# Kernel optimization log

Measured on AMD Instinct MI355X. Metric: run time of the kernel, lower is better.

## Reference

```python
import jax, jax.numpy as jnp
import numpy as np

HEADS = 12
DIM_HEAD = 64
SCALE = DIM_HEAD ** -0.5


def rotate_every_two(x):
    # (..., 2d) -> rotate pairs: (x1, x2) -> (-x2, x1)
    x = x.reshape(*x.shape[:-1], -1, 2)
    x1, x2 = x[..., 0], x[..., 1]
    return jnp.stack((-x2, x1), axis=-1).reshape(*x.shape[:-2], -1)


def apply_rotary_pos_emb(q, k, sinu_pos):
    # sinu_pos: (b, p, 2c) -> sin, cos each (b, p, c)
    b, p, two_c = sinu_pos.shape
    sp = sinu_pos.reshape(b, p, 2, two_c // 2)
    sin, cos = sp[:, :, 0, :], sp[:, :, 1, :]
    # interleave-repeat to (b, 1, p, 2c) to broadcast over heads
    sin = jnp.repeat(sin, 2, axis=-1)[:, None, :, :]
    cos = jnp.repeat(cos, 2, axis=-1)[:, None, :, :]
    rot = lambda t: t * cos + rotate_every_two(t) * sin
    return rot(q), rot(k)


def setup_inputs() -> dict:
    key = jax.random.key(0)
    ks = jax.random.split(key, 5)
    b, n, dim = 8, 1024, 768
    inner = HEADS * DIM_HEAD
    x = jax.random.normal(ks[0], (b, n, dim), dtype=jnp.float32)
    pos_emb = jax.random.normal(ks[1], (1, n, DIM_HEAD), dtype=jnp.float32)
    W_qkv = jax.random.normal(ks[2], (dim, 3 * inner), dtype=jnp.float32) * (dim ** -0.5)
    W_out = jax.random.normal(ks[3], (inner, dim), dtype=jnp.float32) * (inner ** -0.5)
    b_out = jnp.zeros((dim,), dtype=jnp.float32)
    return {"x": x, "pos_emb": pos_emb, "W_qkv": W_qkv, "W_out": W_out, "b_out": b_out}


def reference(x, pos_emb, W_qkv, W_out, b_out):
    b, n, _ = x.shape
    qkv = x @ W_qkv                                   # (b, n, 3*inner)
    q, k, v = jnp.split(qkv, 3, axis=-1)
    split_heads = lambda t: t.reshape(b, n, HEADS, DIM_HEAD).transpose(0, 2, 1, 3)
    q, k, v = split_heads(q), split_heads(k), split_heads(v)   # (b, h, n, d)
    q, k = apply_rotary_pos_emb(q, k, pos_emb)
    dots = jnp.einsum('bhid,bhjd->bhij', q, k) * SCALE
    attn = jax.nn.softmax(dots, axis=-1)
    out = jnp.einsum('bhij,bhjd->bhid', attn, v)
    out = out.transpose(0, 2, 1, 3).reshape(b, n, HEADS * DIM_HEAD)
    out = out @ W_out + b_out
    return out  # context is None -> torch code returns (out[:, :n], None); n == full length
```

## Files before the change

kernel.cpp:

```cpp
#include <hip/hip_runtime.h>
#include <hip/hip_bf16.h>

typedef __attribute__((ext_vector_type(8))) short bf16x8;
typedef __attribute__((ext_vector_type(4))) float f32x4;
typedef __attribute__((ext_vector_type(4))) unsigned short u16x4;
typedef unsigned short u16;
typedef unsigned int u32;

#define DEVINL __device__ __forceinline__

DEVINL u16 f2bf(float f) {
    union { float f; u32 u; } v; v.f = f;
    u32 r = v.u + 0x7FFFu + ((v.u >> 16) & 1u);
    return (u16)(r >> 16);
}
DEVINL float bf2f(u16 h) {
    union { u32 u; float f; } v; v.u = ((u32)h) << 16;
    return v.f;
}
DEVINL u32 cvt_pk_bf16(float lo, float hi) {
    u32 r;
    asm("v_cvt_pk_bf16_f32 %0, %1, %2" : "=v"(r) : "v"(lo), "v"(hi));
    return r;
}

template<int Nv> DEVINL void vmcnt_asm() {
    if constexpr (Nv == 0) asm volatile("s_waitcnt vmcnt(0)" ::: "memory");
    else if constexpr (Nv == 1) asm volatile("s_waitcnt vmcnt(1)" ::: "memory");
    else if constexpr (Nv == 2) asm volatile("s_waitcnt vmcnt(2)" ::: "memory");
    else if constexpr (Nv == 3) asm volatile("s_waitcnt vmcnt(3)" ::: "memory");
    else if constexpr (Nv == 4) asm volatile("s_waitcnt vmcnt(4)" ::: "memory");
    else if constexpr (Nv == 5) asm volatile("s_waitcnt vmcnt(5)" ::: "memory");
    else if constexpr (Nv == 6) asm volatile("s_waitcnt vmcnt(6)" ::: "memory");
    else asm volatile("s_waitcnt vmcnt(7)" ::: "memory");
}

#define GLOAD_LDS16(g, l) __builtin_amdgcn_global_load_lds( \
    (const __attribute__((address_space(1))) void*)(g), \
    (__attribute__((address_space(3))) void*)(l), 16, 0, 0)

#define SBAR() do { \
    __builtin_amdgcn_sched_barrier(0); \
    __builtin_amdgcn_s_barrier(); \
    __builtin_amdgcn_sched_barrier(0); } while (0)

__global__ void cvt_bf16_kernel(const float* __restrict__ in, u16* __restrict__ out, int n4) {
    int t = blockIdx.x * blockDim.x + threadIdx.x;
    if (t >= n4) return;
    const float4 v = reinterpret_cast<const float4*>(in)[t];
    u16x4 o;
    o[0] = f2bf(v.x); o[1] = f2bf(v.y); o[2] = f2bf(v.z); o[3] = f2bf(v.w);
    *reinterpret_cast<u16x4*>(out + (size_t)t * 4) = o;
}

__global__ __launch_bounds__(256) void transpose_cvt_kernel(const float* __restrict__ in,
                                                            u16* __restrict__ out,
                                                            int R, int C) {
    __shared__ float tile[32][33];
    int c0 = blockIdx.x * 32, r0 = blockIdx.y * 32;
    int tx = threadIdx.x & 31, ty = threadIdx.x >> 5;
#pragma unroll
    for (int i = 0; i < 4; ++i)
        tile[ty + i * 8][tx] = in[(size_t)(r0 + ty + i * 8) * C + c0 + tx];
    __syncthreads();
#pragma unroll
    for (int i = 0; i < 4; ++i)
        out[(size_t)(c0 + ty + i * 8) * R + r0 + tx] = f2bf(tile[tx][ty + i * 8]);
}

template<int NTN, int NFRAG, int BROWS, int K, bool BF16_OUT>
__global__ __launch_bounds__(512, 2) void gemm_bigtile_kernel(const u16* __restrict__ A,
                                                              const u16* __restrict__ Bt,
                                                              void* __restrict__ Cout,
                                                              const float* __restrict__ bias) {
    constexpr int BN = NFRAG * 32;
    constexpr int N = NTN * BN;
    constexpr int NT = K / 64;
    constexpr int PA = 256 * 32;
    constexpr int PB = BROWS * 32;
    constexpr int PKS = PA + PB;
    constexpr int PBUF = 2 * PKS;
    constexpr int BFULL = (BROWS * 4) / 512;
    constexpr int BREM = (BROWS * 4) % 512;
    __shared__ u16 lds[2 * PBUF];

    const int tid = threadIdx.x;
    const int wv = tid >> 6, lane = tid & 63;
    const int lr = lane & 15, lg = lane >> 4;
    const int wr = wv >> 1, wc = wv & 1;

    const int id = blockIdx.x;
    const int sid = (id & 7) * 32 + (id >> 3);
    const int bm = (sid / NTN) * 256;
    const int bn = (sid % NTN) * BN;

#define PL(buf_, ks_, mat_) ((buf_) * PBUF + (ks_) * PKS + (mat_) * PA)

#define STAGE_A(nb_, kt_, ks_) do { \
    _Pragma("unroll") \
    for (int j_ = 0; j_ < 2; ++j_) { \
        const int idx_ = j_ * 512 + tid; \
        const int row_ = idx_ >> 2; \
        const int c_ = (idx_ & 3) ^ ((row_ >> 1) & 3); \
        GLOAD_LDS16(A + (size_t)(bm + row_) * K + (kt_) * 64 + (ks_) * 32 + c_ * 8, \
                    (char*)lds + PL((nb_), (ks_), 0) * 2 + j_ * 8192 + tid * 16); \
    } } while (0)

#define STAGE_B(nb_, kt_, ks_) do { \
    _Pragma("unroll") \
    for (int j_ = 0; j_ < BFULL; ++j_) { \
        const int idx_ = j_ * 512 + tid; \
        const int row_ = idx_ >> 2; \
        const int c_ = (idx_ & 3) ^ ((row_ >> 1) & 3); \
        GLOAD_LDS16(Bt + (size_t)(bn + row_) * K + (kt_) * 64 + (ks_) * 32 + c_ * 8, \
                    (char*)lds + PL((nb_), (ks_), 1) * 2 + j_ * 8192 + tid * 16); \
    } \
    if constexpr (BREM != 0) { \
        if (tid < BREM) { \
            const int idx_ = BFULL * 512 + tid; \
            const int row_ = idx_ >> 2; \
            const int c_ = (idx_ & 3) ^ ((row_ >> 1) & 3); \
            GLOAD_LDS16(Bt + (size_t)(bn + row_) * K + (kt_) * 64 + (ks_) * 32 + c_ * 8, \
                        (char*)lds + PL((nb_), (ks_), 1) * 2 + BFULL * 8192 + tid * 16); \
        } \
    } } while (0)

#define LDA(mh_, ks_, cur_) do { \
    _Pragma("unroll") \
    for (int f_ = 0; f_ < 2; ++f_) { \
        const int row_ = wr * 64 + (mh_) * 32 + f_ * 16 + lr; \
        af[f_] = *reinterpret_cast<const bf16x8*>( \
            &lds[PL((cur_), (ks_), 0) + row_ * 32 + ((lg ^ ((row_ >> 1) & 3)) << 3)]); \
    } } while (0)

#define LDB(ks_, cur_) do { \
    _Pragma("unroll") \
    for (int nf_ = 0; nf_ < NFRAG; ++nf_) { \
        const int row_ = wc * (NFRAG * 16) + nf_ * 16 + lr; \
        bfr[nf_] = *reinterpret_cast<const bf16x8*>( \
            &lds[PL((cur_), (ks_), 1) + row_ * 32 + ((lg ^ ((row_ >> 1) & 3)) << 3)]); \
    } } while (0)

#define MFMAQ(mh_) do { \
    __builtin_amdgcn_s_setprio(1); \
    _Pragma("unroll") \
    for (int f_ = 0; f_ < 2; ++f_) \
    _Pragma("unroll") \
    for (int nf_ = 0; nf_ < NFRAG; ++nf_) \
        acc[(mh_) * 2 + f_][nf_] = __builtin_amdgcn_mfma_f32_16x16x32_bf16( \
            af[f_], bfr[nf_], acc[(mh_) * 2 + f_][nf_], 0, 0, 0); \
    __builtin_amdgcn_s_setprio(0); } while (0)

#define WAITHALF() do { \
    __builtin_amdgcn_sched_barrier(0); \
    if constexpr (BREM != 0) { \
        if (wv < BREM / 64) vmcnt_asm<2 + BFULL + 1>(); \
        else vmcnt_asm<2 + BFULL>(); \
    } else { \
        vmcnt_asm<2 + BFULL>(); \
    } } while (0)

    f32x4 acc[4][NFRAG];
#pragma unroll
    for (int i = 0; i < 4; ++i)
#pragma unroll
        for (int j = 0; j < NFRAG; ++j) acc[i][j] = (f32x4){0.f, 0.f, 0.f, 0.f};

    bf16x8 af[2], bfr[NFRAG];

    STAGE_A(0, 0, 0); STAGE_B(0, 0, 0); STAGE_A(0, 0, 1); STAGE_B(0, 0, 1);
    __builtin_amdgcn_sched_barrier(0);
    vmcnt_asm<0>();
    SBAR();

    for (int kt = 0; kt < NT - 1; ++kt) {
        const int cur = kt & 1, nxt = cur ^ 1;
        LDB(0, cur); LDA(0, 0, cur);
        STAGE_A(nxt, kt + 1, 0);
        SBAR(); MFMAQ(0); SBAR();
        LDA(1, 0, cur);
        STAGE_B(nxt, kt + 1, 0);
        WAITHALF();
        SBAR(); MFMAQ(1); SBAR();
        LDB(1, cur); LDA(0, 1, cur);
        STAGE_A(nxt, kt + 1, 1);
        SBAR(); MFMAQ(0); SBAR();
        LDA(1, 1, cur);
        STAGE_B(nxt, kt + 1, 1);
        WAITHALF();
        SBAR(); MFMAQ(1); SBAR();
    }
    {
        const int cur = (NT - 1) & 1;
        LDB(0, cur); LDA(0, 0, cur); SBAR(); MFMAQ(0); SBAR();
        LDA(1, 0, cur);
        __builtin_amdgcn_sched_barrier(0);
        vmcnt_asm<0>();
        SBAR(); MFMAQ(1); SBAR();
        LDB(1, cur); LDA(0, 1, cur); SBAR(); MFMAQ(0); SBAR();
        LDA(1, 1, cur); SBAR(); MFMAQ(1);
    }

#pragma unroll
    for (int mf = 0; mf < 4; ++mf)
#pragma unroll
        for (int nf = 0; nf < NFRAG; ++nf) {
            const int col = bn + wc * (NFRAG * 16) + nf * 16 + lr;
            const float bv = BF16_OUT ? 0.f : bias[col];
#pragma unroll
            for (int r = 0; r < 4; ++r) {
                const int row = bm + wr * 64 + mf * 16 + lg * 4 + r;
                if (BF16_OUT)
                    ((u16*)Cout)[(size_t)row * N + col] = f2bf(acc[mf][nf][r]);
                else
                    ((float*)Cout)[(size_t)row * N + col] = acc[mf][nf][r] + bv;
            }
        }
#undef PL
#undef STAGE_A
#undef STAGE_B
#undef LDA
#undef LDB
#undef MFMAQ
#undef WAITHALF
}

__global__ __launch_bounds__(256) void rot_vtrans_kernel(u16* __restrict__ qkv,
                                                         const float* __restrict__ pos,
                                                         u16* __restrict__ Vt) {
    __shared__ u16 tile[64][72];
    const int bid = blockIdx.x;
    if (bid < 6144) {
        int t = bid * 256 + threadIdx.x;
        int row = t / 192;
        int col = (t % 192) * 8;
        int n = row & 1023;
        int i0 = (col & 63) >> 1;
        const float qs = (col < 768) ? 0.18033688f : 1.0f;
        const float* pn = pos + (size_t)n * 64;
        u16* p = qkv + (size_t)row * 2304 + col;
        bf16x8 v = *reinterpret_cast<bf16x8*>(p);
        u16 o[8];
#pragma unroll
        for (int j = 0; j < 4; ++j) {
            float s = pn[i0 + j], c = pn[32 + i0 + j];
            float x0 = bf2f((u16)v[2 * j]), x1 = bf2f((u16)v[2 * j + 1]);
            o[2 * j]     = f2bf((x0 * c - x1 * s) * qs);
            o[2 * j + 1] = f2bf((x1 * c + x0 * s) * qs);
        }
        *reinterpret_cast<bf16x8*>(p) = *reinterpret_cast<bf16x8*>(o);
    } else {
        int u = bid - 6144;
        int nt = u & 15;
        int bh = u >> 4;
        int b = bh / 12, h = bh % 12;
        int tid = threadIdx.x;
        int rr = tid >> 3, cc = (tid & 7) * 8;
#pragma unroll
        for (int it = 0; it < 2; ++it) {
            int nloc = it * 32 + rr;
            const u16* src = qkv + (size_t)(b * 1024 + nt * 64 + nloc) * 2304 + 1536 + h * 64 + cc;
            bf16x8 v = *reinterpret_cast<const bf16x8*>(src);
#pragma unroll
            for (int j = 0; j < 8; ++j) tile[nloc][cc + j] = (u16)v[j];
        }
        __syncthreads();
#pragma unroll
        for (int it = 0; it < 2; ++it) {
            int d = it * 32 + rr;
            u16 o[8];
#pragma unroll
            for (int j = 0; j < 8; ++j) o[j] = tile[cc + j][d];
            *reinterpret_cast<bf16x8*>(Vt + (size_t)(bh * 64 + d) * 1024 + nt * 64 + cc) =
                *reinterpret_cast<bf16x8*>(o);
        }
    }
}

__global__ __launch_bounds__(512, 8) void attn_kernel(const u16* __restrict__ qkv,
                                                      const u16* __restrict__ Vt,
                                                      u16* __restrict__ attn_out) {
    __shared__ u16 Ks[2][64 * 64];
    __shared__ u16 Vs[2][64 * 64];
    const int d_ = blockIdx.x;
    const int bh = ((d_ >> 3) >> 3) * 8 + (d_ & 7);
    const int qt = (d_ >> 3) & 7;
    const int b = bh / 12, h = bh % 12;
    const int tid = threadIdx.x;
    const int w = tid >> 6, lr = tid & 15, lg = (tid >> 4) & 3;

    bf16x8 qf[2];
#pragma unroll
    for (int ds = 0; ds < 2; ++ds)
        qf[ds] = *reinterpret_cast<const bf16x8*>(
            &qkv[(size_t)(b * 1024 + qt * 128 + w * 16 + lr) * 2304 + h * 64 + ds * 32 + lg * 8]);

    f32x4 o[4];
#pragma unroll
    for (int i = 0; i < 4; ++i) o[i] = (f32x4){0.f, 0.f, 0.f, 0.f};
    float lsum = 0.f;

    const int srow = tid >> 3;
    const int scol = ((tid & 7) ^ (srow & 7)) * 8;
    const int srowK = (srow & 0x20) | ((srow & 0x0C) << 1) | ((srow & 0x10) >> 2) | (srow & 3);

#define STAGE_KV(nb, kt_) do { \
    GLOAD_LDS16(qkv + (size_t)(b * 1024 + (kt_) * 64 + srowK) * 2304 + 768 + h * 64 + scol, \
                (char*)Ks[nb] + tid * 16); \
    GLOAD_LDS16(Vt + (size_t)(bh * 64 + srow) * 1024 + (kt_) * 64 + scol, \
                (char*)Vs[nb] + tid * 16); \
} while (0)

    STAGE_KV(0, 0);
    __syncthreads();

    const int rsw = lr & 7;

    for (int kt = 0; kt < 16; ++kt) {
        const int cur = kt & 1;
        if (kt < 15) STAGE_KV(cur ^ 1, kt + 1);

        f32x4 s[4];
        __builtin_amdgcn_s_setprio(1);
#pragma unroll
        for (int kf = 0; kf < 4; ++kf) {
            f32x4 acc = (f32x4){0.f, 0.f, 0.f, 0.f};
#pragma unroll
            for (int ds = 0; ds < 2; ++ds) {
                bf16x8 kfr = *reinterpret_cast<const bf16x8*>(
                    &Ks[cur][(kf * 16 + lr) * 64 + (((ds * 4 + lg) ^ rsw) * 8)]);
                acc = __builtin_amdgcn_mfma_f32_16x16x32_bf16(kfr, qf[ds], acc, 0, 0, 0);
            }
            s[kf] = acc;
        }
        __builtin_amdgcn_s_setprio(0);

#pragma unroll
        for (int kf = 0; kf < 4; ++kf)
#pragma unroll
            for (int r = 0; r < 4; ++r) s[kf][r] = __builtin_amdgcn_exp2f(s[kf][r]);
        {
            float t0 = (s[0][0] + s[0][1]) + (s[0][2] + s[0][3]);
            float t1 = (s[1][0] + s[1][1]) + (s[1][2] + s[1][3]);
            float t2 = (s[2][0] + s[2][1]) + (s[2][2] + s[2][3]);
            float t3 = (s[3][0] + s[3][1]) + (s[3][2] + s[3][3]);
            lsum += (t0 + t1) + (t2 + t3);
        }

        union { u32 wd[4]; bf16x8 v; } pk[2];
#pragma unroll
        for (int ks = 0; ks < 2; ++ks) {
            pk[ks].wd[0] = cvt_pk_bf16(s[2 * ks][0], s[2 * ks][1]);
            pk[ks].wd[1] = cvt_pk_bf16(s[2 * ks][2], s[2 * ks][3]);
            pk[ks].wd[2] = cvt_pk_bf16(s[2 * ks + 1][0], s[2 * ks + 1][1]);
            pk[ks].wd[3] = cvt_pk_bf16(s[2 * ks + 1][2], s[2 * ks + 1][3]);
        }

        __builtin_amdgcn_s_setprio(1);
#pragma unroll
        for (int ks = 0; ks < 2; ++ks) {
#pragma unroll
            for (int df = 0; df < 4; ++df) {
                bf16x8 vb = *reinterpret_cast<const bf16x8*>(
                    &Vs[cur][(df * 16 + lr) * 64 + (((ks * 4 + lg) ^ rsw) * 8)]);
                o[df] = __builtin_amdgcn_mfma_f32_16x16x32_bf16(vb, pk[ks].v, o[df], 0, 0, 0);
            }
        }
        __builtin_amdgcn_s_setprio(0);
        __syncthreads();
    }
#undef STAGE_KV

    lsum += __shfl_xor(lsum, 16);
    lsum += __shfl_xor(lsum, 32);
    const float linv = 1.0f / lsum;

    u16* orow = attn_out + (size_t)(b * 1024 + qt * 128 + w * 16 + lr) * 768 + h * 64 + lg * 4;
#pragma unroll
    for (int df = 0; df < 4; ++df) {
        uint2 st;
        st.x = cvt_pk_bf16(o[df][0] * linv, o[df][1] * linv);
        st.y = cvt_pk_bf16(o[df][2] * linv, o[df][3] * linv);
        *reinterpret_cast<uint2*>(orow + df * 16) = st;
    }
}

extern "C" void kernel_launch(void* const* d_in, const int* in_sizes, int n_in,
                              void* d_out, int out_size, void* d_ws, size_t ws_size,
                              hipStream_t stream) {
    (void)in_sizes; (void)n_in; (void)out_size; (void)ws_size;
    const float* x     = (const float*)d_in[0];
    const float* pos   = (const float*)d_in[1];
    const float* W_qkv = (const float*)d_in[2];
    const float* W_out = (const float*)d_in[3];
    const float* b_out = (const float*)d_in[4];
    float* out = (float*)d_out;

    char* ws = (char*)d_ws;
    u16* xb     = (u16*)(ws);
    u16* Wqkv_t = (u16*)(ws + 12582912);
    u16* Wout_t = (u16*)(ws + 16171008);
    u16* qkv    = (u16*)(ws + 17399808);
    u16* Vt     = (u16*)(ws + 55148544);
    u16* attn_o = (u16*)(ws + 67731456);

    cvt_bf16_kernel<<<6144, 256, 0, stream>>>(x, xb, 1572864);
    transpose_cvt_kernel<<<dim3(72, 24), 256, 0, stream>>>(W_qkv, Wqkv_t, 768, 2304);
    transpose_cvt_kernel<<<dim3(24, 24), 256, 0, stream>>>(W_out, Wout_t, 768, 768);
    gemm_bigtile_kernel<8, 9, 320, 768, true><<<256, 512, 0, stream>>>(xb, Wqkv_t, qkv, nullptr);
    rot_vtrans_kernel<<<7680, 256, 0, stream>>>(qkv, pos, Vt);
    attn_kernel<<<768, 512, 0, stream>>>(qkv, Vt, attn_o);
    gemm_bigtile_kernel<8, 3, 128, 768, false><<<256, 512, 0, stream>>>(attn_o, Wout_t, out, b_out);
}
```

Measured before the change: 115.3 us.

## Fuse input prep kernels and replace QKV GEMM with smaller-tile kernel

Merges the x conversion and both weight transpose-conversions into a single launch with block-index dispatch, which removes launch overhead. It also replaces the big-tile QKV GEMM (256 blocks of 512 threads) with a new 128x192-tile, K-step-32 double-buffered kernel that runs 768 blocks of 256 threads. The new GEMM uses an XOR-swizzled LDS layout, direct global-to-LDS loads and a grid remap meant to improve locality. The intent is better occupancy and load balance across CUs, at the cost of less operand reuse per tile and scalar bf16 stores in the epilogue.

```diff
diff --git a/kernel.cpp b/kernel.cpp
--- a/kernel.cpp
+++ b/kernel.cpp
@@ -26,13 +26,11 @@
 
 template<int Nv> DEVINL void vmcnt_asm() {
     if constexpr (Nv == 0) asm volatile("s_waitcnt vmcnt(0)" ::: "memory");
-    else if constexpr (Nv == 1) asm volatile("s_waitcnt vmcnt(1)" ::: "memory");
-    else if constexpr (Nv == 2) asm volatile("s_waitcnt vmcnt(2)" ::: "memory");
     else if constexpr (Nv == 3) asm volatile("s_waitcnt vmcnt(3)" ::: "memory");
-    else if constexpr (Nv == 4) asm volatile("s_waitcnt vmcnt(4)" ::: "memory");
     else if constexpr (Nv == 5) asm volatile("s_waitcnt vmcnt(5)" ::: "memory");
     else if constexpr (Nv == 6) asm volatile("s_waitcnt vmcnt(6)" ::: "memory");
-    else asm volatile("s_waitcnt vmcnt(7)" ::: "memory");
+    else if constexpr (Nv == 7) asm volatile("s_waitcnt vmcnt(7)" ::: "memory");
+    else asm volatile("s_waitcnt vmcnt(4)" ::: "memory");
 }
 
 #define GLOAD_LDS16(g, l) __builtin_amdgcn_global_load_lds( \
@@ -44,20 +42,33 @@
     __builtin_amdgcn_s_barrier(); \
     __builtin_amdgcn_sched_barrier(0); } while (0)
 
-__global__ void cvt_bf16_kernel(const float* __restrict__ in, u16* __restrict__ out, int n4) {
-    int t = blockIdx.x * blockDim.x + threadIdx.x;
-    if (t >= n4) return;
-    const float4 v = reinterpret_cast<const float4*>(in)[t];
-    u16x4 o;
-    o[0] = f2bf(v.x); o[1] = f2bf(v.y); o[2] = f2bf(v.z); o[3] = f2bf(v.w);
-    *reinterpret_cast<u16x4*>(out + (size_t)t * 4) = o;
-}
-
-__global__ __launch_bounds__(256) void transpose_cvt_kernel(const float* __restrict__ in,
-                                                            u16* __restrict__ out,
-                                                            int R, int C) {
+__global__ __launch_bounds__(256) void prep_kernel(const float* __restrict__ x,
+                                                   u16* __restrict__ xb,
+                                                   const float* __restrict__ W_qkv,
+                                                   u16* __restrict__ Wqkv_t,
+                                                   const float* __restrict__ W_out,
+                                                   u16* __restrict__ Wout_t) {
     __shared__ float tile[32][33];
-    int c0 = blockIdx.x * 32, r0 = blockIdx.y * 32;
+    const int bid = blockIdx.x;
+    if (bid < 3072) {
+        int t = bid * 256 + threadIdx.x;
+        const float4 v0 = reinterpret_cast<const float4*>(x)[t * 2];
+        const float4 v1 = reinterpret_cast<const float4*>(x)[t * 2 + 1];
+        u16 o[8];
+        o[0] = f2bf(v0.x); o[1] = f2bf(v0.y); o[2] = f2bf(v0.z); o[3] = f2bf(v0.w);
+        o[4] = f2bf(v1.x); o[5] = f2bf(v1.y); o[6] = f2bf(v1.z); o[7] = f2bf(v1.w);
+        *reinterpret_cast<bf16x8*>(xb + (size_t)t * 8) = *reinterpret_cast<bf16x8*>(o);
+        return;
+    }
+    const float* in; u16* out; int R, C, bx, by;
+    if (bid < 4800) {
+        int u = bid - 3072; in = W_qkv; out = Wqkv_t; R = 768; C = 2304;
+        bx = u % 72; by = u / 72;
+    } else {
+        int u = bid - 4800; in = W_out; out = Wout_t; R = 768; C = 768;
+        bx = u % 24; by = u / 24;
+    }
+    int c0 = bx * 32, r0 = by * 32;
     int tx = threadIdx.x & 31, ty = threadIdx.x >> 5;
 #pragma unroll
     for (int i = 0; i < 4; ++i)
@@ -66,6 +77,103 @@
 #pragma unroll
     for (int i = 0; i < 4; ++i)
         out[(size_t)(c0 + ty + i * 8) * R + r0 + tx] = f2bf(tile[tx][ty + i * 8]);
+}
+
+template<int K>
+__global__ __launch_bounds__(256, 3) void gemm1_kernel(const u16* __restrict__ A,
+                                                       const u16* __restrict__ Bt,
+                                                       u16* __restrict__ Cout) {
+    constexpr int NT = K / 32;
+    constexpr int PBUF = (128 + 192) * 32;
+    __shared__ u16 lds[2 * PBUF];
+
+    const int tid = threadIdx.x;
+    const int wv = tid >> 6, lane = tid & 63;
+    const int lr = lane & 15, lg = lane >> 4;
+    const int wr = wv >> 1, wc = wv & 1;
+
+    const int id = blockIdx.x;
+    const int sid = (id & 7) * 96 + (id >> 3);
+    const int bm = (sid / 12) * 128;
+    const int bn = (sid % 12) * 192;
+
+#define STAGE(nb_, kt_) do { \
+    _Pragma("unroll") \
+    for (int j_ = 0; j_ < 2; ++j_) { \
+        const int idx_ = j_ * 256 + tid; \
+        const int row_ = idx_ >> 2; \
+        const int c_ = (idx_ & 3) ^ ((row_ >> 1) & 3); \
+        GLOAD_LDS16(A + (size_t)(bm + row_) * K + (kt_) * 32 + c_ * 8, \
+                    (char*)lds + (nb_) * (PBUF * 2) + j_ * 4096 + tid * 16); \
+    } \
+    _Pragma("unroll") \
+    for (int j_ = 0; j_ < 3; ++j_) { \
+        const int idx_ = j_ * 256 + tid; \
+        const int row_ = idx_ >> 2; \
+        const int c_ = (idx_ & 3) ^ ((row_ >> 1) & 3); \
+        GLOAD_LDS16(Bt + (size_t)(bn + row_) * K + (kt_) * 32 + c_ * 8, \
+                    (char*)lds + (nb_) * (PBUF * 2) + 8192 + j_ * 4096 + tid * 16); \
+    } } while (0)
+
+    f32x4 acc[4][6];
+#pragma unroll
+    for (int i = 0; i < 4; ++i)
+#pragma unroll
+        for (int j = 0; j < 6; ++j) acc[i][j] = (f32x4){0.f, 0.f, 0.f, 0.f};
+
+    STAGE(0, 0);
+    __builtin_amdgcn_sched_barrier(0);
+    vmcnt_asm<0>();
+    SBAR();
+
+    for (int kt = 0; kt < NT; ++kt) {
+        const int cur = kt & 1;
+        if (kt < NT - 1) {
+            STAGE(cur ^ 1, kt + 1);
+            __builtin_amdgcn_sched_barrier(0);
+            vmcnt_asm<5>();
+            SBAR();
+        } else {
+            __builtin_amdgcn_sched_barrier(0);
+            vmcnt_asm<0>();
+            SBAR();
+        }
+        bf16x8 af[4], bfr[6];
+#pragma unroll
+        for (int mf = 0; mf < 4; ++mf) {
+            const int row = wr * 64 + mf * 16 + lr;
+            af[mf] = *reinterpret_cast<const bf16x8*>(
+                &lds[cur * PBUF + row * 32 + ((lg ^ ((row >> 1) & 3)) << 3)]);
+        }
+#pragma unroll
+        for (int nf = 0; nf < 6; ++nf) {
+            const int row = wc * 96 + nf * 16 + lr;
+            bfr[nf] = *reinterpret_cast<const bf16x8*>(
+                &lds[cur * PBUF + 4096 + row * 32 + ((lg ^ ((row >> 1) & 3)) << 3)]);
+        }
+        __builtin_amdgcn_s_setprio(1);
+#pragma unroll
+        for (int mf = 0; mf < 4; ++mf)
+#pragma unroll
+            for (int nf = 0; nf < 6; ++nf)
+                acc[mf][nf] = __builtin_amdgcn_mfma_f32_16x16x32_bf16(
+                    af[mf], bfr[nf], acc[mf][nf], 0, 0, 0);
+        __builtin_amdgcn_s_setprio(0);
+        SBAR();
+    }
+
+#pragma unroll
+    for (int mf = 0; mf < 4; ++mf)
+#pragma unroll
+        for (int nf = 0; nf < 6; ++nf) {
+            const int col = bn + wc * 96 + nf * 16 + lr;
+#pragma unroll
+            for (int r = 0; r < 4; ++r) {
+                const int row = bm + wr * 64 + mf * 16 + lg * 4 + r;
+                Cout[(size_t)row * 2304 + col] = f2bf(acc[mf][nf][r]);
+            }
+        }
+#undef STAGE
 }
 
 template<int NTN, int NFRAG, int BROWS, int K, bool BF16_OUT>
@@ -404,10 +512,8 @@
     u16* Vt     = (u16*)(ws + 55148544);
     u16* attn_o = (u16*)(ws + 67731456);
 
-    cvt_bf16_kernel<<<6144, 256, 0, stream>>>(x, xb, 1572864);
-    transpose_cvt_kernel<<<dim3(72, 24), 256, 0, stream>>>(W_qkv, Wqkv_t, 768, 2304);
-    transpose_cvt_kernel<<<dim3(24, 24), 256, 0, stream>>>(W_out, Wout_t, 768, 768);
-    gemm_bigtile_kernel<8, 9, 320, 768, true><<<256, 512, 0, stream>>>(xb, Wqkv_t, qkv, nullptr);
+    prep_kernel<<<5376, 256, 0, stream>>>(x, xb, W_qkv, Wqkv_t, W_out, Wout_t);
+    gemm1_kernel<768><<<768, 256, 0, stream>>>(xb, Wqkv_t, qkv);
     rot_vtrans_kernel<<<7680, 256, 0, stream>>>(qkv, pos, Vt);
     attn_kernel<<<768, 512, 0, stream>>>(qkv, Vt, attn_o);
     gemm_bigtile_kernel<8, 3, 128, 768, false><<<256, 512, 0, stream>>>(attn_o, Wout_t, out, b_out);
```

Measured after the change: 113.7 us. Within noise of the previous version (-1.4%).
